# Optimization experiments

Hardware: AMD Instinct MI355X
Metric: run time of the kernel (lower is better)

The kernel has to match this reference:

```python
import jax, jax.numpy as jnp
from jax import lax
import numpy as np

SEQ_LEN = 2048
BATCH = 512
HIDDEN = 256
CLASSES = 10


def setup_inputs() -> dict:
    key = jax.random.key(0)
    k1, k2, k3, k4 = jax.random.split(key, 4)
    return {
        "x": jax.random.normal(k1, (BATCH, SEQ_LEN), dtype=jnp.float32),
        "W_hx": jax.random.normal(k2, (HIDDEN, 1), dtype=jnp.float32),
        "W_hh": jax.random.normal(k3, (HIDDEN, HIDDEN), dtype=jnp.float32),
        "W_ph": jax.random.normal(k4, (CLASSES, HIDDEN), dtype=jnp.float32),
        "bias_h": jnp.zeros((HIDDEN, 1), dtype=jnp.float32),
        "bias_p": jnp.zeros((CLASSES,), dtype=jnp.float32),
    }


def reference(x, W_hx, W_hh, W_ph, bias_h, bias_p):
    # x: [B, T]. Hidden state h: [H, B]. Only last-step p is returned,
    # matching the torch loop where p is overwritten each iteration.
    B = x.shape[0]
    h0 = jnp.zeros((W_hh.shape[0], B), dtype=x.dtype)

    def step(h, x_t):  # x_t: [B]
        # W_hx @ x_t[None,:] : [H,1]@[1,B] -> [H,B]
        h_new = jnp.tanh(W_hx @ x_t[None, :] + W_hh @ h + bias_h)
        return h_new, None

    h_T, _ = lax.scan(step, h0, x.T)  # scan over time: x.T is [T, B]
    p = h_T.T @ W_ph.T + bias_p  # [B, C]
    return p
```

## Files before the change

### kernel.cpp

```cpp
#include <hip/hip_runtime.h>
#include <math.h>


#define TT 2048
#define BB 512
#define HH 256
#define CC 10
#define KH 128

__device__ __forceinline__ float ref_tanhf(float x)
{
    const float a1  = 4.89352455891786e-03f;
    const float a3  = 6.37261928875436e-04f;
    const float a5  = 1.48572235717979e-05f;
    const float a7  = 5.12229709037114e-08f;
    const float a9  = -8.60467152213735e-11f;
    const float a11 = 2.00018790482477e-13f;
    const float a13 = -2.76076847742355e-16f;
    const float b0  = 4.89352518554385e-03f;
    const float b2  = 2.26843463243900e-03f;
    const float b4  = 1.18534705686654e-04f;
    const float b6  = 1.19825839466702e-06f;

    const float kClamp = 7.99881172180175781f;
    const float xc = fmaxf(fminf(x, kClamp), -kClamp);
    const float x2 = __fmul_rn(xc, xc);
    float p = fmaf(x2, a13, a11);
    p = fmaf(x2, p, a9);
    p = fmaf(x2, p, a7);
    p = fmaf(x2, p, a5);
    p = fmaf(x2, p, a3);
    p = fmaf(x2, p, a1);
    p = __fmul_rn(xc, p);
    float q = fmaf(x2, b6, b4);
    q = fmaf(x2, q, b2);
    q = fmaf(x2, q, b0);
    const float r = __fdiv_rn(p, q);
    return (fabsf(x) < 0.0004f) ? x : r;
}

__global__ __launch_bounds__(512, 2)
void rnn_fwd(const float* __restrict__ x,
             const float* __restrict__ W_hx,
             const float* __restrict__ W_hh,
             const float* __restrict__ W_ph,
             const float* __restrict__ bias_h,
             const float* __restrict__ bias_p,
             float* __restrict__ out)
{
    const int tid   = threadIdx.x;
    const int group = tid >> 8;
    const int i     = tid & (HH - 1);
    const int b0    = blockIdx.x * 2;

    __shared__ __align__(16) float xls[2][TT];
    __shared__ __align__(16) float hbuf[2][2][HH];
    __shared__ __align__(16) float zpart[2][HH];

    float w[KH];
    const float* __restrict__ wrow = W_hh + (size_t)i * HH + group * KH;
#pragma unroll
    for (int k = 0; k < KH; k += 4) {
        const float4 v = *reinterpret_cast<const float4*>(wrow + k);
        w[k] = v.x; w[k + 1] = v.y; w[k + 2] = v.z; w[k + 3] = v.w;
    }
#pragma unroll
    for (int k = 0; k < KH; ++k) {
        asm volatile("" : "+v"(w[k]));
    }

    {
        const float4* __restrict__ xsrc =
            reinterpret_cast<const float4*>(x + (size_t)b0 * TT);
        float4* __restrict__ xdst = reinterpret_cast<float4*>(&xls[0][0]);
        xdst[tid]       = xsrc[tid];
        xdst[512 + tid] = xsrc[512 + tid];
    }
    const float whx = W_hx[i];
    const float bh  = bias_h[i];

    hbuf[group][1][i] = 0.0f;
    __syncthreads();

#define PBODY(COL, T, RP)                                                     \
    {                                                                         \
        const float* __restrict__ h = &hbuf[(COL)][(RP)][0];                  \
        float z = 0.0f;                                                       \
        _Pragma("unroll")                                                     \
        for (int k = 0; k < KH; k += 4) {                                     \
            const float4 h4 = *reinterpret_cast<const float4*>(h + k);        \
            z = fmaf(w[k],     h4.x, z);                                      \
            z = fmaf(w[k + 1], h4.y, z);                                      \
            z = fmaf(w[k + 2], h4.z, z);                                      \
            z = fmaf(w[k + 3], h4.w, z);                                      \
        }                                                                     \
        zpart[(COL)][i] = z;                                                  \
    }

#define QBODY(COL, T, RP)                                                     \
    {                                                                         \
        const float* __restrict__ h = &hbuf[(COL)][(RP)][0];                  \
        float z = zpart[(COL)][i];                                            \
        _Pragma("unroll")                                                     \
        for (int k = 0; k < KH; k += 4) {                                     \
            const float4 h4 = *reinterpret_cast<const float4*>(h + KH + k);   \
            z = fmaf(w[k],     h4.x, z);                                      \
            z = fmaf(w[k + 1], h4.y, z);                                      \
            z = fmaf(w[k + 2], h4.z, z);                                      \
            z = fmaf(w[k + 3], h4.w, z);                                      \
        }                                                                     \
        const float a0 = __fmul_rn(whx, xls[(COL)][(T)]);                     \
        z = __fadd_rn(__fadd_rn(a0, z), bh);                                  \
        hbuf[(COL)][(RP) ^ 1][i] = ref_tanhf(z);                              \
    }

#define STEP(U, RP)                                                           \
    {                                                                         \
        if (group == 0) { PBODY(0, (U), (RP)) }                               \
        else if ((U) >= 1) { QBODY(1, (U) - 1, (RP) ^ 1) }                    \
        __syncthreads();                                                      \
        if (group == 0) { PBODY(1, (U), (RP)) }                               \
        else { QBODY(0, (U), (RP)) }                                          \
        __syncthreads();                                                      \
    }

    STEP(0, 1)
    for (int u = 1; u + 1 < TT; u += 2) {
        STEP(u, 0)
        STEP(u + 1, 1)
    }
    STEP(TT - 1, 0)
    if (group == 1) { QBODY(1, TT - 1, 0) }
    __syncthreads();

#undef STEP
#undef QBODY
#undef PBODY

    if (tid < 2 * CC) {
        const int col = tid / CC;
        const int c   = tid % CC;
        const float* __restrict__ wp = W_ph + (size_t)c * HH;
        const float* __restrict__ hf = hbuf[col][1];
        float pv = 0.0f;
#pragma unroll 8
        for (int k = 0; k < HH; ++k) {
            pv = fmaf(hf[k], wp[k], pv);
        }
        out[(size_t)(b0 + col) * CC + c] = __fadd_rn(pv, bias_p[c]);
    }
}

extern "C" void kernel_launch(void* const* d_in, const int* in_sizes, int n_in,
                              void* d_out, int out_size, void* d_ws, size_t ws_size,
                              hipStream_t stream) {
    const float* x      = (const float*)d_in[0];
    const float* W_hx   = (const float*)d_in[1];
    const float* W_hh   = (const float*)d_in[2];
    const float* W_ph   = (const float*)d_in[3];
    const float* bias_h = (const float*)d_in[4];
    const float* bias_p = (const float*)d_in[5];
    float* out = (float*)d_out;

    rnn_fwd<<<dim3(BB / 2), dim3(512), 0, stream>>>(x, W_hx, W_hh, W_ph, bias_h, bias_p, out);
}
```

Before: 3.049 ms.

## Split recurrent matvec into four-stage K pipeline with two rows per thread

Reorganises each block's hidden-state matvec. The reduction dimension is now split into four 64-wide slices owned by four 128-thread groups, and each thread handles two hidden rows, giving two interleaved FMA chains. The two batch columns are staggered so groups work on different stages at once, with partial sums passed through three shared-memory buffers. This shortens each dependent FMA chain and adds ILP, but each time step now needs four barriers instead of two, and only half the threads are active in each phase.

```diff
diff --git a/kernel.cpp b/kernel.cpp
--- a/kernel.cpp
+++ b/kernel.cpp
@@ -6,7 +6,7 @@
 #define BB 512
 #define HH 256
 #define CC 10
-#define KH 128
+#define KH 64
 
 __device__ __forceinline__ float ref_tanhf(float x)
 {
@@ -49,24 +49,32 @@
              float* __restrict__ out)
 {
     const int tid   = threadIdx.x;
-    const int group = tid >> 8;
-    const int i     = tid & (HH - 1);
+    const int group = tid >> 7;
+    const int r     = tid & 127;
     const int b0    = blockIdx.x * 2;
 
     __shared__ __align__(16) float xls[2][TT];
     __shared__ __align__(16) float hbuf[2][2][HH];
-    __shared__ __align__(16) float zpart[2][HH];
-
-    float w[KH];
-    const float* __restrict__ wrow = W_hh + (size_t)i * HH + group * KH;
+    __shared__ __align__(16) float zb0[2][HH];
+    __shared__ __align__(16) float zb1[2][HH];
+    __shared__ __align__(16) float zb2[2][HH];
+
+    float wa[KH], wb[KH];
+    {
+        const float* __restrict__ wra = W_hh + (size_t)r * HH + group * KH;
+        const float* __restrict__ wrb = W_hh + (size_t)(r + 128) * HH + group * KH;
 #pragma unroll
-    for (int k = 0; k < KH; k += 4) {
-        const float4 v = *reinterpret_cast<const float4*>(wrow + k);
-        w[k] = v.x; w[k + 1] = v.y; w[k + 2] = v.z; w[k + 3] = v.w;
+        for (int k = 0; k < KH; k += 4) {
+            const float4 va = *reinterpret_cast<const float4*>(wra + k);
+            wa[k] = va.x; wa[k + 1] = va.y; wa[k + 2] = va.z; wa[k + 3] = va.w;
+            const float4 vb = *reinterpret_cast<const float4*>(wrb + k);
+            wb[k] = vb.x; wb[k + 1] = vb.y; wb[k + 2] = vb.z; wb[k + 3] = vb.w;
+        }
     }
 #pragma unroll
     for (int k = 0; k < KH; ++k) {
-        asm volatile("" : "+v"(w[k]));
+        asm volatile("" : "+v"(wa[k]));
+        asm volatile("" : "+v"(wb[k]));
     }
 
     {
@@ -76,66 +84,108 @@
         xdst[tid]       = xsrc[tid];
         xdst[512 + tid] = xsrc[512 + tid];
     }
-    const float whx = W_hx[i];
-    const float bh  = bias_h[i];
-
-    hbuf[group][1][i] = 0.0f;
+    const float whxa = W_hx[r];
+    const float whxb = W_hx[r + 128];
+    const float bha  = bias_h[r];
+    const float bhb  = bias_h[r + 128];
+
+    if (tid < 256)      hbuf[0][1][tid] = 0.0f;
+    else                hbuf[1][1][tid - 256] = 0.0f;
     __syncthreads();
 
-#define PBODY(COL, T, RP)                                                     \
+#define CHAIN4(ZA, ZB, W_A, W_B, H4, K)                                       \
+    ZA = fmaf(W_A[(K)],     H4.x, ZA);  ZB = fmaf(W_B[(K)],     H4.x, ZB);    \
+    ZA = fmaf(W_A[(K) + 1], H4.y, ZA);  ZB = fmaf(W_B[(K) + 1], H4.y, ZB);    \
+    ZA = fmaf(W_A[(K) + 2], H4.z, ZA);  ZB = fmaf(W_B[(K) + 2], H4.z, ZB);    \
+    ZA = fmaf(W_A[(K) + 3], H4.w, ZA);  ZB = fmaf(W_B[(K) + 3], H4.w, ZB);
+
+#define S0B(COL, RP)                                                          \
     {                                                                         \
         const float* __restrict__ h = &hbuf[(COL)][(RP)][0];                  \
-        float z = 0.0f;                                                       \
-        _Pragma("unroll")                                                     \
-        for (int k = 0; k < KH; k += 4) {                                     \
-            const float4 h4 = *reinterpret_cast<const float4*>(h + k);        \
-            z = fmaf(w[k],     h4.x, z);                                      \
-            z = fmaf(w[k + 1], h4.y, z);                                      \
-            z = fmaf(w[k + 2], h4.z, z);                                      \
-            z = fmaf(w[k + 3], h4.w, z);                                      \
-        }                                                                     \
-        zpart[(COL)][i] = z;                                                  \
-    }
-
-#define QBODY(COL, T, RP)                                                     \
-    {                                                                         \
-        const float* __restrict__ h = &hbuf[(COL)][(RP)][0];                  \
-        float z = zpart[(COL)][i];                                            \
-        _Pragma("unroll")                                                     \
-        for (int k = 0; k < KH; k += 4) {                                     \
-            const float4 h4 = *reinterpret_cast<const float4*>(h + KH + k);   \
-            z = fmaf(w[k],     h4.x, z);                                      \
-            z = fmaf(w[k + 1], h4.y, z);                                      \
-            z = fmaf(w[k + 2], h4.z, z);                                      \
-            z = fmaf(w[k + 3], h4.w, z);                                      \
-        }                                                                     \
-        const float a0 = __fmul_rn(whx, xls[(COL)][(T)]);                     \
-        z = __fadd_rn(__fadd_rn(a0, z), bh);                                  \
-        hbuf[(COL)][(RP) ^ 1][i] = ref_tanhf(z);                              \
-    }
-
-#define STEP(U, RP)                                                           \
-    {                                                                         \
-        if (group == 0) { PBODY(0, (U), (RP)) }                               \
-        else if ((U) >= 1) { QBODY(1, (U) - 1, (RP) ^ 1) }                    \
-        __syncthreads();                                                      \
-        if (group == 0) { PBODY(1, (U), (RP)) }                               \
-        else { QBODY(0, (U), (RP)) }                                          \
-        __syncthreads();                                                      \
-    }
-
-    STEP(0, 1)
-    for (int u = 1; u + 1 < TT; u += 2) {
-        STEP(u, 0)
-        STEP(u + 1, 1)
-    }
-    STEP(TT - 1, 0)
-    if (group == 1) { QBODY(1, TT - 1, 0) }
+        float za = 0.0f, zv = 0.0f;                                           \
+        _Pragma("unroll")                                                     \
+        for (int j = 0; j < KH; j += 4) {                                     \
+            const float4 h4 = *reinterpret_cast<const float4*>(h + j);        \
+            CHAIN4(za, zv, wa, wb, h4, j)                                     \
+        }                                                                     \
+        zb0[(COL)][r] = za;  zb0[(COL)][r + 128] = zv;                        \
+    }
+
+#define S1B(COL, RP)                                                          \
+    {                                                                         \
+        const float* __restrict__ h = &hbuf[(COL)][(RP)][KH];                 \
+        float za = zb0[(COL)][r], zv = zb0[(COL)][r + 128];                   \
+        _Pragma("unroll")                                                     \
+        for (int j = 0; j < KH; j += 4) {                                     \
+            const float4 h4 = *reinterpret_cast<const float4*>(h + j);        \
+            CHAIN4(za, zv, wa, wb, h4, j)                                     \
+        }                                                                     \
+        zb1[(COL)][r] = za;  zb1[(COL)][r + 128] = zv;                        \
+    }
+
+#define S2B(COL, RP)                                                          \
+    {                                                                         \
+        const float* __restrict__ h = &hbuf[(COL)][(RP)][2 * KH];             \
+        float za = zb1[(COL)][r], zv = zb1[(COL)][r + 128];                   \
+        _Pragma("unroll")                                                     \
+        for (int j = 0; j < KH; j += 4) {                                     \
+            const float4 h4 = *reinterpret_cast<const float4*>(h + j);        \
+            CHAIN4(za, zv, wa, wb, h4, j)                                     \
+        }                                                                     \
+        zb2[(COL)][r] = za;  zb2[(COL)][r + 128] = zv;                        \
+    }
+
+#define S3B(COL, RPX, T)                                                      \
+    {                                                                         \
+        const float* __restrict__ h = &hbuf[(COL)][(RPX)][3 * KH];            \
+        float za = zb2[(COL)][r], zv = zb2[(COL)][r + 128];                   \
+        _Pragma("unroll")                                                     \
+        for (int j = 0; j < KH; j += 4) {                                     \
+            const float4 h4 = *reinterpret_cast<const float4*>(h + j);        \
+            CHAIN4(za, zv, wa, wb, h4, j)                                     \
+        }                                                                     \
+        const float xt = xls[(COL)][(T)];                                     \
+        const float aa = __fmul_rn(whxa, xt);                                 \
+        const float ab = __fmul_rn(whxb, xt);                                 \
+        za = __fadd_rn(__fadd_rn(aa, za), bha);                               \
+        zv = __fadd_rn(__fadd_rn(ab, zv), bhb);                               \
+        hbuf[(COL)][(RPX) ^ 1][r]       = ref_tanhf(za);                      \
+        hbuf[(COL)][(RPX) ^ 1][r + 128] = ref_tanhf(zv);                      \
+    }
+
+#define STEP(T, WP, RP, HD)                                                   \
+    {                                                                         \
+        if (group == 0) { S0B(0, RP) }                                        \
+        else if (!(HD) && group == 2) { S2B(1, WP) }                          \
+        __syncthreads();                                                      \
+        if (group == 1) { S1B(0, RP) }                                        \
+        else if (!(HD) && group == 3) { S3B(1, WP, (T) - 1) }                 \
+        __syncthreads();                                                      \
+        if (group == 2) { S2B(0, RP) }                                        \
+        else if (group == 0) { S0B(1, RP) }                                   \
+        __syncthreads();                                                      \
+        if (group == 3) { S3B(0, RP, T) }                                     \
+        else if (group == 1) { S1B(1, RP) }                                   \
+        __syncthreads();                                                      \
+    }
+
+    STEP(0, 0, 1, 1)
+    STEP(1, 1, 0, 0)
+    for (int t = 2; t < TT; t += 2) {
+        STEP(t, 0, 1, 0)
+        STEP(t + 1, 1, 0, 0)
+    }
+    if (group == 2) { S2B(1, 0) }
     __syncthreads();
+    if (group == 3) { S3B(1, 0, TT - 1) }
+    __syncthreads();
 
 #undef STEP
-#undef QBODY
-#undef PBODY
+#undef S3B
+#undef S2B
+#undef S1B
+#undef S0B
+#undef CHAIN4
 
     if (tid < 2 * CC) {
         const int col = tid / CC;
```

Result: slower. 4.661 ms (+52.9%).

## Replace block barriers with per-column LDS flag spin-waits between producer/consumer groups

Applied to the files above, without the earlier changes.

The two block-wide barriers per step are replaced by a point-to-point handshake through shared-memory counters. Group 0 computes the first half of each dot product and bumps a per-column counter; group 1 spins on that counter, finishes the step, applies tanh and bumps a second counter for the next step. The partial-sum buffer is double-buffered so the two groups can drift further apart. This aims to remove barrier stalls and let the groups pipeline independently, but it adds busy-wait polling that uses issue slots and LDS bandwidth, and its correctness relies on fence and atomic ordering.

```diff
diff --git a/kernel.cpp b/kernel.cpp
--- a/kernel.cpp
+++ b/kernel.cpp
@@ -51,11 +51,14 @@
     const int tid   = threadIdx.x;
     const int group = tid >> 8;
     const int i     = tid & (HH - 1);
+    const int lane  = tid & 63;
     const int b0    = blockIdx.x * 2;
 
     __shared__ __align__(16) float xls[2][TT];
     __shared__ __align__(16) float hbuf[2][2][HH];
-    __shared__ __align__(16) float zpart[2][HH];
+    __shared__ __align__(16) float zpart[2][2][HH];
+    __shared__ int zdone[2];
+    __shared__ int hdone[2];
 
     float w[KH];
     const float* __restrict__ wrow = W_hh + (size_t)i * HH + group * KH;
@@ -80,10 +83,24 @@
     const float bh  = bias_h[i];
 
     hbuf[group][1][i] = 0.0f;
+    if (tid == 0) { zdone[0] = 0; zdone[1] = 0; hdone[0] = 0; hdone[1] = 0; }
     __syncthreads();
 
-#define PBODY(COL, T, RP)                                                     \
+#define ARRIVE(FLAG)                                                          \
     {                                                                         \
+        __threadfence_block();                                                \
+        if (lane == 0) atomicAdd(&(FLAG), 1);                                 \
+    }
+#define SPIN(FLAG, TGT)                                                       \
+    {                                                                         \
+        volatile int* f_ = &(FLAG);                                           \
+        while (*f_ < (TGT)) {}                                                \
+        __threadfence_block();                                                \
+    }
+
+#define PSTEP(COL, U, RP)                                                     \
+    {                                                                         \
+        SPIN(hdone[(COL)], 4 * (U))                                           \
         const float* __restrict__ h = &hbuf[(COL)][(RP)][0];                  \
         float z = 0.0f;                                                       \
         _Pragma("unroll")                                                     \
@@ -94,48 +111,46 @@
             z = fmaf(w[k + 2], h4.z, z);                                      \
             z = fmaf(w[k + 3], h4.w, z);                                      \
         }                                                                     \
-        zpart[(COL)][i] = z;                                                  \
+        zpart[(COL)][(RP) ^ 1][i] = z;                                        \
+        ARRIVE(zdone[(COL)])                                                  \
     }
 
-#define QBODY(COL, T, RP)                                                     \
+#define QSTEP(COL, U, RP)                                                     \
     {                                                                         \
-        const float* __restrict__ h = &hbuf[(COL)][(RP)][0];                  \
-        float z = zpart[(COL)][i];                                            \
+        SPIN(zdone[(COL)], 4 * ((U) + 1))                                     \
+        const float* __restrict__ h = &hbuf[(COL)][(RP)][KH];                 \
+        float z = zpart[(COL)][(RP) ^ 1][i];                                  \
         _Pragma("unroll")                                                     \
         for (int k = 0; k < KH; k += 4) {                                     \
-            const float4 h4 = *reinterpret_cast<const float4*>(h + KH + k);   \
+            const float4 h4 = *reinterpret_cast<const float4*>(h + k);        \
             z = fmaf(w[k],     h4.x, z);                                      \
             z = fmaf(w[k + 1], h4.y, z);                                      \
             z = fmaf(w[k + 2], h4.z, z);                                      \
             z = fmaf(w[k + 3], h4.w, z);                                      \
         }                                                                     \
-        const float a0 = __fmul_rn(whx, xls[(COL)][(T)]);                     \
+        const float a0 = __fmul_rn(whx, xls[(COL)][(U)]);                     \
         z = __fadd_rn(__fadd_rn(a0, z), bh);                                  \
         hbuf[(COL)][(RP) ^ 1][i] = ref_tanhf(z);                              \
+        ARRIVE(hdone[(COL)])                                                  \
     }
 
-#define STEP(U, RP)                                                           \
-    {                                                                         \
-        if (group == 0) { PBODY(0, (U), (RP)) }                               \
-        else if ((U) >= 1) { QBODY(1, (U) - 1, (RP) ^ 1) }                    \
-        __syncthreads();                                                      \
-        if (group == 0) { PBODY(1, (U), (RP)) }                               \
-        else { QBODY(0, (U), (RP)) }                                          \
-        __syncthreads();                                                      \
+    if (group == 0) {
+        for (int u = 0; u < TT; u += 2) {
+            PSTEP(0, u, 1)     PSTEP(1, u, 1)
+            PSTEP(0, u + 1, 0) PSTEP(1, u + 1, 0)
+        }
+    } else {
+        for (int u = 0; u < TT; u += 2) {
+            QSTEP(0, u, 1)     QSTEP(1, u, 1)
+            QSTEP(0, u + 1, 0) QSTEP(1, u + 1, 0)
+        }
     }
-
-    STEP(0, 1)
-    for (int u = 1; u + 1 < TT; u += 2) {
-        STEP(u, 0)
-        STEP(u + 1, 1)
-    }
-    STEP(TT - 1, 0)
-    if (group == 1) { QBODY(1, TT - 1, 0) }
     __syncthreads();
 
-#undef STEP
-#undef QBODY
-#undef PBODY
+#undef QSTEP
+#undef PSTEP
+#undef SPIN
+#undef ARRIVE
 
     if (tid < 2 * CC) {
         const int col = tid / CC;
```

Measured after the change: 3.225 ms. 5.8% more time.
